# Performance work log

Hardware: AMD Instinct MI355X
Metric: run time of the kernel (lower is better)

The kernel has to match this reference:

```python
import jax, jax.numpy as jnp
import numpy as np

B, T, HW = 4, 27, 224
DIM, HEADS, LAYERS, MLP, NCLS, SEQ = 256, 4, 7, 512, 101, 56 * 56
HEAD_DIM = DIM // HEADS


def ste_sign(x):
    # binarize to {-1,0,+1} via sign() with straight-through gradient (matches torch .data mutation)
    return x + jax.lax.stop_gradient(jnp.sign(x) - x)


def layer_norm(x, s, b, eps=1e-5):
    m = x.mean(-1, keepdims=True)
    v = ((x - m) ** 2).mean(-1, keepdims=True)
    return (x - m) / jnp.sqrt(v + eps) * s + b


def conv3d(x, w, stride, pad):
    return jax.lax.conv_general_dilated(x, w, stride, [(p, p) for p in pad],
                                        dimension_numbers=('NCDHW', 'OIDHW', 'NCDHW'))


def encoder_layer(xx, p):
    l1s, l1b, qw, qb, pw, pb, l2s, l2b, f1w, f1b, f2w, f2b = p
    h = layer_norm(xx, l1s, l1b)
    qkv = jnp.einsum('bnd,ed->bne', h, qw) + qb  # (B, SEQ, 3*DIM)
    q, k, v = [t.reshape(B, SEQ, HEADS, HEAD_DIM).transpose(0, 2, 1, 3)
               for t in jnp.split(qkv, 3, axis=-1)]
    attn = jax.nn.softmax(jnp.einsum('bhnd,bhmd->bhnm', q, k) * HEAD_DIM ** -0.5, axis=-1)
    o = jnp.einsum('bhnm,bhmd->bhnd', attn, v).transpose(0, 2, 1, 3).reshape(B, SEQ, DIM)
    xx = xx + jnp.einsum('bnd,ed->bne', o, pw) + pb
    h = layer_norm(xx, l2s, l2b)
    h = jax.nn.gelu(jnp.einsum('bnd,ed->bne', h, f1w) + f1b, approximate=False)
    return xx + jnp.einsum('bne,de->bnd', h, f2w) + f2b, None


def forward(x, w1, w2, w3, tok_w, pos_emb, ln1_s, ln1_b, qkv_w, qkv_b, proj_w, proj_b,
            ln2_s, ln2_b, fc1_w, fc1_b, fc2_w, fc2_b, lnf_s, lnf_b, pool_w, pool_b,
            head_w, head_b, remat=False):
    st, pd = (3, 1, 1), (1, 3, 3)
    # BinarizeConv3d chain: first conv sees raw 3-channel input; later convs binarize their input
    h = jax.nn.relu(conv3d(x, ste_sign(w1), st, pd))            # (B,64,9,224,224)
    h = jax.nn.relu(conv3d(ste_sign(h), ste_sign(w2), st, pd))  # (B,32,3,224,224)
    h = jax.nn.relu(conv3d(ste_sign(h), ste_sign(w3), st, pd))  # (B,3,1,224,224)
    h = h.reshape(B, 3, HW, HW)
    # CCT tokenizer: Conv2d(3,256,k7,s2,p3,bias=False) + ReLU + MaxPool(3,2,1)
    t = jax.nn.relu(jax.lax.conv_general_dilated(h, tok_w, (2, 2), [(3, 3), (3, 3)],
                                                 dimension_numbers=('NCHW', 'OIHW', 'NCHW')))
    t = jax.lax.reduce_window(t, -jnp.inf, jax.lax.max, (1, 1, 3, 3), (1, 1, 2, 2),
                              ((0, 0), (0, 0), (1, 1), (1, 1)))  # (B,256,56,56)
    z = t.reshape(B, DIM, SEQ).transpose(0, 2, 1) + pos_emb      # (B,3136,256)
    body = jax.checkpoint(encoder_layer) if remat else encoder_layer
    z, _ = jax.lax.scan(body, z, (ln1_s, ln1_b, qkv_w, qkv_b, proj_w, proj_b,
                                  ln2_s, ln2_b, fc1_w, fc1_b, fc2_w, fc2_b))
    z = layer_norm(z, lnf_s, lnf_b)
    # sequence pooling: softmax(Linear(dim,1)) over tokens, weighted sum, then classifier
    a = jax.nn.softmax(z @ pool_w + pool_b, axis=1)  # (B, SEQ)
    pooled = jnp.einsum('bn,bnd->bd', a, z)
    return pooled @ head_w.T + head_b                # (B, 101)


def setup_inputs() -> dict:
    key = jax.random.key(0)
    ks = jax.random.split(key, 12)
    r = lambda k, s, sc=0.02: jax.random.normal(k, s, jnp.float32) * sc
    return {
        'x': jax.random.normal(ks[0], (B, 3, T, HW, HW), jnp.float32),
        'w1': r(ks[1], (64, 3, 3, 7, 7), 1.0),
        'w2': r(ks[2], (32, 64, 3, 7, 7), 1.0),
        'w3': r(ks[3], (3, 32, 3, 7, 7), 1.0),
        'tok_w': r(ks[4], (DIM, 3, 7, 7)),
        'pos_emb': r(ks[5], (1, SEQ, DIM), 0.2),
        'ln1_s': jnp.ones((LAYERS, DIM)), 'ln1_b': jnp.zeros((LAYERS, DIM)),
        'qkv_w': r(ks[6], (LAYERS, 3 * DIM, DIM)), 'qkv_b': jnp.zeros((LAYERS, 3 * DIM)),
        'proj_w': r(ks[7], (LAYERS, DIM, DIM)), 'proj_b': jnp.zeros((LAYERS, DIM)),
        'ln2_s': jnp.ones((LAYERS, DIM)), 'ln2_b': jnp.zeros((LAYERS, DIM)),
        'fc1_w': r(ks[8], (LAYERS, MLP, DIM)), 'fc1_b': jnp.zeros((LAYERS, MLP)),
        'fc2_w': r(ks[9], (LAYERS, DIM, MLP)), 'fc2_b': jnp.zeros((LAYERS, DIM)),
        'lnf_s': jnp.ones((DIM,)), 'lnf_b': jnp.zeros((DIM,)),
        'pool_w': r(ks[10], (DIM,)), 'pool_b': jnp.zeros((1,)),
        'head_w': r(ks[11], (NCLS, DIM)), 'head_b': jnp.zeros((NCLS,)),
    }


def reference(x, w1, w2, w3, tok_w, pos_emb, ln1_s, ln1_b, qkv_w, qkv_b, proj_w, proj_b,
              ln2_s, ln2_b, fc1_w, fc1_b, fc2_w, fc2_b, lnf_s, lnf_b, pool_w, pool_b,
              head_w, head_b):
    return forward(x, w1, w2, w3, tok_w, pos_emb, ln1_s, ln1_b, qkv_w, qkv_b, proj_w,
                   proj_b, ln2_s, ln2_b, fc1_w, fc1_b, fc2_w, fc2_b, lnf_s, lnf_b,
                   pool_w, pool_b, head_w, head_b)
```

## Files before the change

kernel.cpp:

```cpp
#include <hip/hip_runtime.h>
#include <hip/hip_bf16.h>
#include <cstdint>

#define SEQL 3136

typedef __attribute__((ext_vector_type(8))) short v8s;
typedef __attribute__((ext_vector_type(4))) float f32x4;
typedef __attribute__((ext_vector_type(4))) int v4i;

__device__ __forceinline__ uint16_t bf16u(float f) {
    uint32_t u = __float_as_uint(f);
    uint32_t r = u + 0x7fff + ((u >> 16) & 1);
    return (uint16_t)(r >> 16);
}
__device__ __forceinline__ float bf2f(uint16_t b) {
    uint32_t u = ((uint32_t)b) << 16;
    return __uint_as_float(u);
}

__global__ __launch_bounds__(256) void k_prep(const float* __restrict__ qw,
                                              const float* __restrict__ pw,
                                              const float* __restrict__ f1,
                                              const float* __restrict__ f2,
                                              const float* __restrict__ w1,
                                              const float* __restrict__ w2,
                                              const float* __restrict__ w3,
                                              uint16_t* __restrict__ dq,
                                              uint16_t* __restrict__ dp,
                                              uint16_t* __restrict__ d1,
                                              uint16_t* __restrict__ d2,
                                              uint16_t* __restrict__ w1b,
                                              uint64_t* __restrict__ wp2,
                                              uint64_t* __restrict__ wn2,
                                              uint32_t* __restrict__ wp3,
                                              uint32_t* __restrict__ wn3,
                                              uint32_t* __restrict__ w2i,
                                              uint16_t* __restrict__ w1f) {
    int gid = blockIdx.x * 256 + threadIdx.x;
    if (gid < 1376256) { dq[gid] = bf16u(qw[gid]); return; }
    if (gid < 1835008) { int i = gid - 1376256; dp[i] = bf16u(pw[i]); return; }
    if (gid < 2752512) { int i = gid - 1835008; d1[i] = bf16u(f1[i]); return; }
    if (gid < 3670016) { int i = gid - 2752512; d2[i] = bf16u(f2[i]); return; }
    if (gid < 3698688) {
        int i = gid - 3670016;
        int c = i & 63, oc = (i >> 6) & 63, kw = i >> 12;
        uint16_t v = 0;
        if (c < 63) {
            int ic = c / 21, rem = c % 21, kd = rem / 7, kh = rem % 7;
            float w = w1[((((oc * 3 + ic) * 3 + kd) * 7 + kh) * 7) + kw];
            v = (w > 0.f) ? 0x3F80 : ((w < 0.f) ? 0xBF80 : 0);
        }
        w1b[i] = v;
        return;
    }
    if (gid < 3703392) {
        int i = gid - 3698688;
        int oc = i / 147, r = i % 147;
        uint64_t p = 0, n = 0;
        for (int ic = 0; ic < 64; ic++) {
            float v = w2[(long)oc * 9408 + (long)ic * 147 + r];
            if (v > 0.f) p |= (1ull << ic);
            else if (v < 0.f) n |= (1ull << ic);
        }
        wp2[i] = p; wn2[i] = n;
        return;
    }
    if (gid < 3703833) {
        int i = gid - 3703392;
        int oc = i / 147, r = i % 147;
        uint32_t p = 0, n = 0;
        for (int ic = 0; ic < 32; ic++) {
            float v = w3[(long)oc * 4704 + (long)ic * 147 + r];
            if (v > 0.f) p |= (1u << ic);
            else if (v < 0.f) n |= (1u << ic);
        }
        wp3[i] = p; wn3[i] = n;
        return;
    }
    if (gid < 3779097) {
        int j = gid - 3703833;
        int s4 = (j & 3) * 4;
        int lane = (j >> 2) & 63;
        int nt = (j >> 8) & 1;
        int r = j >> 9;
        int g = lane >> 4, tl = lane & 15;
        int oc = nt * 16 + tl;
        uint32_t out = 0;
        for (int bb = 0; bb < 4; bb++) {
            int ic = g * 16 + s4 + bb;
            float w = w2[(long)oc * 9408 + (long)ic * 147 + r];
            uint32_t s8 = (w > 0.f) ? 0x01u : ((w < 0.f) ? 0xFFu : 0x00u);
            out |= s8 << (8 * bb);
        }
        w2i[j] = out;
        return;
    }
    if (gid < 3807769) {
        int i = gid - 3779097;
        int e = i & 7;
        int lane = (i >> 3) & 63;
        int f = (i >> 9) & 1;
        int wn = (i >> 10) & 1;
        int ks = (i >> 11) & 1;
        int kw = i >> 12;
        int tl = lane & 15, g = lane >> 4;
        int oc = wn * 32 + f * 16 + tl;
        int c = ks * 32 + g * 8 + e;
        uint16_t v = 0;
        if (c < 63) {
            int ic = c / 21, rem = c % 21, kd = rem / 7, kh = rem % 7;
            float w = w1[((((oc * 3 + ic) * 3 + kd) * 7 + kh) * 7) + kw];
            v = (w > 0.f) ? 0x3F80 : ((w < 0.f) ? 0xBF80 : 0);
        }
        w1f[i] = v;
    }
}

__global__ __launch_bounds__(256) void k_prepx(const float* __restrict__ x,
                                               uint32_t* __restrict__ X3) {
    int gid = blockIdx.x * 256 + threadIdx.x;
    if (gid >= 26158464) return;
    int iwp = gid % 116;
    int t = gid / 116;
    int ihp = t % 232; t /= 232;
    int dslot = t % 27; t /= 27;
    int ic = t % 3; t /= 3;
    int b = t & 3; int s = t >> 2;
    int d = dslot - 1;
    int ih = ihp - 3;
    uint32_t out = 0;
    if (d >= 0 && (unsigned)ih < 224u) {
        const float* xp = x + ((long)(b * 3 + ic) * 27 + d) * 50176 + ih * 224;
#pragma unroll
        for (int half = 0; half < 2; half++) {
            int iw = 2 * iwp + half - 3;
            float v = ((unsigned)iw < 224u) ? xp[iw] : 0.f;
            uint16_t hi = bf16u(v);
            uint16_t o = hi;
            if (s > 0) {
                float r1 = v - bf2f(hi);
                uint16_t lo = bf16u(r1);
                o = (s == 2) ? bf16u(r1 - bf2f(lo)) : lo;
            }
            out |= ((uint32_t)o) << (16 * half);
        }
    }
    X3[gid] = out;
}

__device__ __forceinline__ v8s ldA76(const uint16_t* Xt, int colb, int c0) {
    union { v8s v; uint2 u[2]; } t;
    const uint16_t* p = Xt + colb * 76 + c0;
    t.u[0] = *(const uint2*)p;
    t.u[1] = *(const uint2*)(p + 4);
    return t.v;
}

__global__ __launch_bounds__(256) void k_conv1m(const uint16_t* __restrict__ X3,
                                                const uint16_t* __restrict__ w1f,
                                                uint64_t* __restrict__ b1p) {
    __shared__ __align__(16) uint16_t Xt[232 * 76];
    __shared__ __align__(16) uint16_t Wb[2][4096];
    int tid = threadIdx.x;
    int bidx = blockIdx.x;
    int oh = (bidx & 7) * 28 + (bidx >> 3);
    int od = blockIdx.y, b = blockIdx.z;
    int lane = tid & 63, wv = tid >> 6;
    int wm = wv >> 1, wn = wv & 1;
    int tl = lane & 15, g = lane >> 4;

    f32x4 acc[7][2];
#pragma unroll
    for (int mt = 0; mt < 7; mt++) {
        acc[mt][0] = (f32x4){0.f, 0.f, 0.f, 0.f};
        acc[mt][1] = (f32x4){0.f, 0.f, 0.f, 0.f};
    }

    for (int s = 0; s < 3; s++) {
        if (tid < 232) {
            const uint16_t* Xb = X3 + ((long)(s * 4 + b) * 81 + (long)od * 3) * 53824
                               + oh * 232 + tid;
#pragma unroll
            for (int cp = 0; cp < 32; cp++) {
                const int c0 = 2 * cp, c1 = c0 + 1;
                uint32_t v0 = 0, v1 = 0;
                if (c0 < 63) {
                    const int ickd = c0 / 7, kh = c0 % 7;
                    const int ic = ickd / 3, kd = ickd % 3;
                    v0 = Xb[(long)(ic * 27 + kd) * 53824 + kh * 232];
                }
                if (c1 < 63) {
                    const int ickd = c1 / 7, kh = c1 % 7;
                    const int ic = ickd / 3, kd = ickd % 3;
                    v1 = Xb[(long)(ic * 27 + kd) * 53824 + kh * 232];
                }
                *(uint32_t*)&Xt[tid * 76 + c0] = v0 | (v1 << 16);
            }
        }
        {
            const uint4* src = (const uint4*)w1f;
            uint4* dst = (uint4*)Wb[0];
            dst[tid] = src[tid];
            dst[256 + tid] = src[256 + tid];
        }
        __syncthreads();
        for (int kw = 0; kw < 7; kw++) {
            int cur = kw & 1;
            if (kw < 6) {
                const uint4* src = (const uint4*)(w1f + (kw + 1) * 4096);
                uint4* dst = (uint4*)Wb[cur ^ 1];
                dst[tid] = src[tid];
                dst[256 + tid] = src[256 + tid];
            }
#pragma unroll
            for (int ks = 0; ks < 2; ks++) {
                const uint16_t* wfb = &Wb[cur][((ks * 2 + wn) * 2) * 512 + lane * 8];
                v8s b0 = *(const v8s*)wfb;
                v8s b1 = *(const v8s*)(wfb + 512);
#pragma unroll
                for (int mt = 0; mt < 7; mt++) {
                    int colb = (wm * 7 + mt) * 16 + tl + kw;
                    v8s a = ldA76(Xt, colb, ks * 32 + g * 8);
                    acc[mt][0] = __builtin_amdgcn_mfma_f32_16x16x32_bf16(a, b0, acc[mt][0], 0, 0, 0);
                    acc[mt][1] = __builtin_amdgcn_mfma_f32_16x16x32_bf16(a, b1, acc[mt][1], 0, 0, 0);
                }
            }
            __syncthreads();
        }
    }
    uint16_t* obits16 = (uint16_t*)Wb[1];
#pragma unroll
    for (int mt = 0; mt < 7; mt++)
#pragma unroll
        for (int nt = 0; nt < 2; nt++)
#pragma unroll
            for (int r = 0; r < 4; r++) {
                unsigned long long mask = __ballot(acc[mt][nt][r] > 0.f);
                if (tl == 0) {
                    int ow = (wm * 7 + mt) * 16 + g * 4 + r;
                    obits16[ow * 4 + wn * 2 + nt] = (uint16_t)(mask >> (g * 16));
                }
            }
    __syncthreads();
    if (tid < 224) {
        uint64_t w = (uint64_t)obits16[tid * 4]
                   | ((uint64_t)obits16[tid * 4 + 1] << 16)
                   | ((uint64_t)obits16[tid * 4 + 2] << 32)
                   | ((uint64_t)obits16[tid * 4 + 3] << 48);
        b1p[(((long)b * 9 + od) * 224 + oh) * 224 + tid] = w;
    }
}

__global__ __launch_bounds__(256) void k_conv2m(const uint64_t* __restrict__ bp1,
                                                const uint8_t* __restrict__ w2i,
                                                uint32_t* __restrict__ b2p) {
    __shared__ __align__(16) uint64_t xs[21 * 232];
    __shared__ uint16_t obits16[224 * 2];
    int tid = threadIdx.x;
    int bidx = blockIdx.x;
    int oh = (bidx & 7) * 28 + (bidx >> 3);
    int od = blockIdx.y, b = blockIdx.z;
    int lane = tid & 63, wv = tid >> 6;
    int tl = lane & 15, g = lane >> 4;
    int g2 = g >> 1, sh = (g & 1) * 16;

    for (int i = tid; i < 21 * 232; i += 256) {
        int row = i / 232, wp = i - row * 232;
        int kd = row / 7, kh = row - kd * 7;
        int d = od * 3 - 1 + kd;
        int h = oh - 3 + kh;
        int w = wp - 3;
        uint64_t v = 0;
        if ((unsigned)d < 9u && (unsigned)h < 224u && (unsigned)w < 224u)
            v = bp1[(((long)b * 9 + d) * 224 + h) * 224 + w];
        xs[i] = v;
    }

    int nmt = (wv < 2) ? 4 : 3;
    v4i acc[4][2];
#pragma unroll
    for (int mi = 0; mi < 4; mi++) {
        acc[mi][0] = (v4i){0, 0, 0, 0};
        acc[mi][1] = (v4i){0, 0, 0, 0};
    }
    __syncthreads();

    for (int row = 0; row < 21; row++) {
        const uint8_t* wr = w2i + (long)row * 14336;
        const uint32_t* x32 = (const uint32_t*)&xs[row * 232];
#pragma unroll
        for (int kw = 0; kw < 7; kw++) {
            v4i bf0 = *(const v4i*)&wr[(kw * 2 + 0) * 1024 + lane * 16];
            v4i bf1 = *(const v4i*)&wr[(kw * 2 + 1) * 1024 + lane * 16];
#pragma unroll
            for (int mi = 0; mi < 4; mi++) {
                if (mi < nmt) {
                    int mt = wv + mi * 4;
                    uint32_t c = x32[(mt * 16 + tl + kw) * 2 + g2] >> sh;
                    v4i a;
#pragma unroll
                    for (int j = 0; j < 4; j++) {
                        uint32_t d4 = (c >> (4 * j)) & 0xFu;
                        a[j] = (int)((d4 * 0x204081u) & 0x01010101u);
                    }
                    acc[mi][0] = __builtin_amdgcn_mfma_i32_16x16x64_i8(a, bf0, acc[mi][0], 0, 0, 0);
                    acc[mi][1] = __builtin_amdgcn_mfma_i32_16x16x64_i8(a, bf1, acc[mi][1], 0, 0, 0);
                }
            }
        }
    }
#pragma unroll
    for (int mi = 0; mi < 4; mi++) {
        if (mi < nmt) {
            int mt = wv + mi * 4;
#pragma unroll
            for (int nt = 0; nt < 2; nt++)
#pragma unroll
                for (int r = 0; r < 4; r++) {
                    unsigned long long mask = __ballot(acc[mi][nt][r] > 0);
                    if (tl == 0)
                        obits16[(mt * 16 + g * 4 + r) * 2 + nt] = (uint16_t)(mask >> (g * 16));
                }
        }
    }
    __syncthreads();
    if (tid < 224) {
        uint32_t wo = (uint32_t)obits16[tid * 2] | ((uint32_t)obits16[tid * 2 + 1] << 16);
        b2p[(((long)b * 3 + od) * 224 + oh) * 224 + tid] = wo;
    }
}

__global__ __launch_bounds__(256) void k_conv3(const uint32_t* __restrict__ bp2,
                                               const uint32_t* __restrict__ wp,
                                               const uint32_t* __restrict__ wn,
                                               float* __restrict__ h3) {
    int gid = blockIdx.x * 256 + threadIdx.x;
    int q = gid;
    int ow = q % 224; q /= 224;
    int oh = q % 224; q /= 224;
    int oc = q % 3;   int b = q / 3;
    int acc = 0;
    for (int kd = 0; kd < 3; kd++) {
        int d = kd - 1;
        if ((unsigned)d >= 3u) continue;
        for (int kh = 0; kh < 7; kh++) {
            int h = oh - 3 + kh;
            if ((unsigned)h >= 224u) continue;
            const uint32_t* bp = bp2 + ((long)(b * 3 + d) * 224 + h) * 224;
            const uint32_t* mp = wp + ((oc * 3 + kd) * 7 + kh) * 7;
            const uint32_t* mn = wn + ((oc * 3 + kd) * 7 + kh) * 7;
#pragma unroll
            for (int kw = 0; kw < 7; kw++) {
                int w = ow - 3 + kw;
                if ((unsigned)w < 224u) {
                    uint32_t bits = bp[w];
                    acc += __popc(bits & mp[kw]) - __popc(bits & mn[kw]);
                }
            }
        }
    }
    h3[gid] = fmaxf((float)acc, 0.f);
}

__global__ __launch_bounds__(256) void k_tok(const float* __restrict__ h3,
                                             const float* __restrict__ wt,
                                             float* __restrict__ tok) {
    __shared__ float xs[3 * 7 * 232];
    int tid = threadIdx.x;
    int oh = blockIdx.x, b = blockIdx.y;
    for (int i = tid; i < 3 * 7 * 232; i += 256) {
        int col = i % 232; int t = i / 232;
        int kh = t % 7; int ic = t / 7;
        int ih = oh * 2 - 3 + kh;
        int iw = col - 3;
        float v = 0.f;
        if ((unsigned)ih < 224u && (unsigned)iw < 224u)
            v = h3[((long)(b * 3 + ic) * 50176) + ih * 224 + iw];
        xs[i] = v;
    }
    __syncthreads();
    int oc = tid;
    float* obase = tok + ((long)(b * 112 + oh) * 112) * 256 + oc;
    for (int chunk = 0; chunk < 4; chunk++) {
        int ow0 = chunk * 28;
        float acc[28];
#pragma unroll
        for (int o2 = 0; o2 < 28; o2++) acc[o2] = 0.f;
        for (int ic = 0; ic < 3; ic++) {
#pragma unroll
            for (int kh = 0; kh < 7; kh++) {
                const float* row = &xs[(ic * 7 + kh) * 232 + ow0 * 2];
                float xv[61];
#pragma unroll
                for (int t = 0; t < 61; t++) xv[t] = row[t];
                const float* wr = wt + (oc * 3 + ic) * 49 + kh * 7;
                float w[7];
#pragma unroll
                for (int kw = 0; kw < 7; kw++) w[kw] = wr[kw];
#pragma unroll
                for (int kw = 0; kw < 7; kw++)
#pragma unroll
                    for (int o2 = 0; o2 < 28; o2++)
                        acc[o2] = fmaf(w[kw], xv[2 * o2 + kw], acc[o2]);
            }
        }
#pragma unroll
        for (int o2 = 0; o2 < 28; o2++)
            obase[(long)(ow0 + o2) * 256] = fmaxf(acc[o2], 0.f);
    }
}

__global__ __launch_bounds__(256) void k_pool_z(const float* __restrict__ tok,
                                                const float* __restrict__ pos,
                                                float* __restrict__ z) {
    int gid = blockIdx.x * 256 + threadIdx.x;
    int c = gid & 255;
    int n = (gid >> 8) % SEQL;
    int b = gid / (256 * SEQL);
    int oh = n / 56, ow = n % 56;
    const float* tp = tok + ((long)b * 112 * 112) * 256 + c;
    float m = -1e30f;
#pragma unroll
    for (int kh = 0; kh < 3; kh++) {
        int h = oh * 2 - 1 + kh;
        if ((unsigned)h >= 112u) continue;
#pragma unroll
        for (int kw = 0; kw < 3; kw++) {
            int w = ow * 2 - 1 + kw;
            if ((unsigned)w < 112u) m = fmaxf(m, tp[(long)(h * 112 + w) * 256]);
        }
    }
    z[gid] = m + pos[n * 256 + c];
}

__global__ __launch_bounds__(256) void k_gemm_ln(const float* __restrict__ Z,
                                                 const uint16_t* __restrict__ W,
                                                 const float* __restrict__ lns,
                                                 const float* __restrict__ lnb,
                                                 const float* __restrict__ bias,
                                                 uint16_t* __restrict__ C,
                                                 uint16_t* __restrict__ VT,
                                                 int N, int dogelu, int dovt) {
    __shared__ uint16_t As[128 * 40], Bs[128 * 40];
    __shared__ float mu[128], rsd[128];
    int tid = threadIdx.x;
    int lane = tid & 63, wave = tid >> 6;
    int wm = wave >> 1, wn = wave & 1;
    int m0 = blockIdx.y * 128, n0 = blockIdx.x * 128;
    {
        int row = tid >> 1, hf = tid & 1;
        const float* zr = Z + (long)(m0 + row) * 256 + hf * 128;
        float s = 0.f, sq = 0.f;
        for (int i = 0; i < 128; i++) { float v = zr[i]; s += v; sq += v * v; }
        s += __shfl_xor(s, 1); sq += __shfl_xor(sq, 1);
        if (hf == 0) {
            float m = s * (1.0f / 256.0f);
            mu[row] = m;
            rsd[row] = rsqrtf(sq * (1.0f / 256.0f) - m * m + 1e-5f);
        }
    }
    f32x4 acc[4][4];
#pragma unroll
    for (int i = 0; i < 4; i++)
#pragma unroll
        for (int j = 0; j < 4; j++) acc[i][j] = (f32x4){0.f, 0.f, 0.f, 0.f};
    int rl = lane & 15, kq = (lane >> 4) * 8;
    for (int k0 = 0; k0 < 256; k0 += 32) {
        __syncthreads();
#pragma unroll
        for (int c2 = 0; c2 < 16; c2++) {
            int idx = c2 * 256 + tid;
            int col = idx & 31, row = idx >> 5;
            float v = Z[(long)(m0 + row) * 256 + k0 + col];
            v = (v - mu[row]) * rsd[row] * lns[k0 + col] + lnb[k0 + col];
            As[row * 40 + col] = bf16u(v);
        }
#pragma unroll
        for (int c = 0; c < 2; c++) {
            int idx = c * 256 + tid;
            int row = idx >> 2, k8 = (idx & 3) * 8;
            *(uint4*)&Bs[row * 40 + k8] = *(const uint4*)&W[(long)(n0 + row) * 256 + k0 + k8];
        }
        __syncthreads();
        v8s a[4], bb[4];
#pragma unroll
        for (int i = 0; i < 4; i++) a[i] = *(const v8s*)&As[(wm * 64 + i * 16 + rl) * 40 + kq];
#pragma unroll
        for (int j = 0; j < 4; j++) bb[j] = *(const v8s*)&Bs[(wn * 64 + j * 16 + rl) * 40 + kq];
#pragma unroll
        for (int i = 0; i < 4; i++)
#pragma unroll
            for (int j = 0; j < 4; j++)
                acc[i][j] = __builtin_amdgcn_mfma_f32_16x16x32_bf16(a[i], bb[j], acc[i][j], 0, 0, 0);
    }
    int rq = (lane >> 4) * 4;
    bool vt = (dovt != 0) && (n0 >= 512);
#pragma unroll
    for (int i = 0; i < 4; i++) {
#pragma unroll
        for (int j = 0; j < 4; j++) {
            int col = n0 + wn * 64 + j * 16 + rl;
            float bval = bias[col];
#pragma unroll
            for (int r = 0; r < 4; r++) {
                int row = m0 + wm * 64 + i * 16 + rq + r;
                float v = acc[i][j][r] + bval;
                if (dogelu) v = 0.5f * v * (1.0f + erff(v * 0.70710678118654752f));
                if (vt) {
                    int hv = col - 512;
                    int h = hv >> 6, d = hv & 63;
                    int bb2 = row / SEQL, nn = row - bb2 * SEQL;
                    VT[((long)(bb2 * 4 + h) * 64 + d) * SEQL + nn] = bf16u(v);
                } else {
                    C[(long)row * N + col] = bf16u(v);
                }
            }
        }
    }
}

__global__ __launch_bounds__(256) void k_gemm(const uint16_t* __restrict__ A,
                                              const uint16_t* __restrict__ W,
                                              const float* __restrict__ bias,
                                              float* __restrict__ C,
                                              int M, int N, int K) {
    __shared__ uint16_t As[128 * 40], Bs[128 * 40];
    int tid = threadIdx.x;
    int lane = tid & 63, wave = tid >> 6;
    int wm = wave >> 1, wn = wave & 1;
    int m0 = blockIdx.y * 128, n0 = blockIdx.x * 128;
    f32x4 acc[4][4];
#pragma unroll
    for (int i = 0; i < 4; i++)
#pragma unroll
        for (int j = 0; j < 4; j++) acc[i][j] = (f32x4){0.f, 0.f, 0.f, 0.f};
    int rl = lane & 15, kq = (lane >> 4) * 8;
    for (int k0 = 0; k0 < K; k0 += 32) {
        __syncthreads();
#pragma unroll
        for (int c = 0; c < 2; c++) {
            int idx = c * 256 + tid;
            int row = idx >> 2, k8 = (idx & 3) * 8;
            *(uint4*)&As[row * 40 + k8] = *(const uint4*)&A[(long)(m0 + row) * K + k0 + k8];
            *(uint4*)&Bs[row * 40 + k8] = *(const uint4*)&W[(long)(n0 + row) * K + k0 + k8];
        }
        __syncthreads();
        v8s a[4], bb[4];
#pragma unroll
        for (int i = 0; i < 4; i++) a[i] = *(const v8s*)&As[(wm * 64 + i * 16 + rl) * 40 + kq];
#pragma unroll
        for (int j = 0; j < 4; j++) bb[j] = *(const v8s*)&Bs[(wn * 64 + j * 16 + rl) * 40 + kq];
#pragma unroll
        for (int i = 0; i < 4; i++)
#pragma unroll
            for (int j = 0; j < 4; j++)
                acc[i][j] = __builtin_amdgcn_mfma_f32_16x16x32_bf16(a[i], bb[j], acc[i][j], 0, 0, 0);
    }
    int rq = (lane >> 4) * 4;
#pragma unroll
    for (int i = 0; i < 4; i++) {
#pragma unroll
        for (int j = 0; j < 4; j++) {
            int col = n0 + wn * 64 + j * 16 + rl;
            float bval = bias[col];
#pragma unroll
            for (int r = 0; r < 4; r++) {
                int row = m0 + wm * 64 + i * 16 + rq + r;
                C[(long)row * N + col] += acc[i][j][r] + bval;
            }
        }
    }
}

__global__ __launch_bounds__(256) void k_flash(const uint16_t* __restrict__ G,
                                               const uint16_t* __restrict__ VT,
                                               uint16_t* __restrict__ o) {
    __shared__ __align__(16) uint32_t Qs[64 * 36], Ks[64 * 36], Vt[64 * 36];
    __shared__ __align__(16) uint16_t Ps[64 * 72];
    int tid = threadIdx.x;
    int lane = tid & 63, wv = tid >> 6;
    int qt = blockIdx.x, h = blockIdx.y, b = blockIdx.z;
    long base = (long)b * SEQL * 768 + h * 64;
    long vtbase = ((long)(b * 4 + h) * 64) * SEQL;
#pragma unroll
    for (int it = 0; it < 2; it++) {
        int idx = it * 256 + tid;
        int q8 = idx & 7, r = idx >> 3;
        *(uint4*)&Qs[r * 36 + q8 * 4] = *(const uint4*)&G[base + (long)(qt * 64 + r) * 768 + q8 * 8];
    }
    int g = lane >> 4, tl = lane & 15;
    int qr0 = wv * 16;
    __syncthreads();
    v8s aq[2];
#pragma unroll
    for (int ks = 0; ks < 2; ks++)
        aq[ks] = *(const v8s*)&Qs[(qr0 + tl) * 36 + ks * 16 + g * 4];

    float m_[4], l_[4];
    f32x4 ov[4];
#pragma unroll
    for (int r = 0; r < 4; r++) { m_[r] = -1e30f; l_[r] = 0.f; }
#pragma unroll
    for (int j = 0; j < 4; j++) ov[j] = (f32x4){0.f, 0.f, 0.f, 0.f};

    for (int kt = 0; kt < 49; kt++) {
        __syncthreads();
#pragma unroll
        for (int it = 0; it < 2; it++) {
            int idx = it * 256 + tid;
            int q8 = idx & 7, r = idx >> 3;
            *(uint4*)&Ks[r * 36 + q8 * 4] =
                *(const uint4*)&G[base + (long)(kt * 64 + r) * 768 + 256 + q8 * 8];
        }
#pragma unroll
        for (int it = 0; it < 2; it++) {
            int idx = it * 256 + tid;
            int r8 = idx & 7, d = idx >> 3;
            *(uint4*)&Vt[d * 36 + r8 * 4] =
                *(const uint4*)&VT[vtbase + (long)d * SEQL + kt * 64 + r8 * 8];
        }
        __syncthreads();
        f32x4 s[4];
#pragma unroll
        for (int j = 0; j < 4; j++) s[j] = (f32x4){0.f, 0.f, 0.f, 0.f};
#pragma unroll
        for (int ks = 0; ks < 2; ks++) {
#pragma unroll
            for (int j = 0; j < 4; j++) {
                v8s bk = *(const v8s*)&Ks[(j * 16 + tl) * 36 + ks * 16 + g * 4];
                s[j] = __builtin_amdgcn_mfma_f32_16x16x32_bf16(aq[ks], bk, s[j], 0, 0, 0);
            }
        }
        float alpha[4];
#pragma unroll
        for (int r = 0; r < 4; r++) {
            float s0 = s[0][r] * 0.125f, s1 = s[1][r] * 0.125f;
            float s2 = s[2][r] * 0.125f, s3 = s[3][r] * 0.125f;
            s[0][r] = s0; s[1][r] = s1; s[2][r] = s2; s[3][r] = s3;
            float mx = fmaxf(fmaxf(s0, s1), fmaxf(s2, s3));
#pragma unroll
            for (int off = 1; off < 16; off <<= 1) mx = fmaxf(mx, __shfl_xor(mx, off));
            float nm = fmaxf(m_[r], mx);
            alpha[r] = __expf(m_[r] - nm);
            float rs = 0.f;
#pragma unroll
            for (int j = 0; j < 4; j++) {
                float p = __expf(s[j][r] - nm);
                s[j][r] = p; rs += p;
            }
#pragma unroll
            for (int off = 1; off < 16; off <<= 1) rs += __shfl_xor(rs, off);
            l_[r] = l_[r] * alpha[r] + rs;
            m_[r] = nm;
        }
#pragma unroll
        for (int j = 0; j < 4; j++)
#pragma unroll
            for (int r = 0; r < 4; r++) ov[j][r] *= alpha[r];
#pragma unroll
        for (int j = 0; j < 4; j++)
#pragma unroll
            for (int r = 0; r < 4; r++)
                Ps[(qr0 + g * 4 + r) * 72 + j * 16 + tl] = bf16u(s[j][r]);
#pragma unroll
        for (int ks = 0; ks < 2; ks++) {
            v8s ap = *(const v8s*)&Ps[(qr0 + tl) * 72 + ks * 32 + g * 8];
#pragma unroll
            for (int jd = 0; jd < 4; jd++) {
                v8s bv = *(const v8s*)&Vt[(jd * 16 + tl) * 36 + ks * 16 + g * 4];
                ov[jd] = __builtin_amdgcn_mfma_f32_16x16x32_bf16(ap, bv, ov[jd], 0, 0, 0);
            }
        }
    }
    long ob = ((long)b * SEQL + qt * 64) * 256 + h * 64;
#pragma unroll
    for (int r = 0; r < 4; r++) {
        float inv = 1.0f / l_[r];
        int row = qr0 + g * 4 + r;
#pragma unroll
        for (int jd = 0; jd < 4; jd++)
            o[ob + (long)row * 256 + jd * 16 + tl] = bf16u(ov[jd][r] * inv);
    }
}

__global__ __launch_bounds__(256) void k_tail_rows(const float* __restrict__ Z,
                                                   const float* __restrict__ g,
                                                   const float* __restrict__ be,
                                                   const float* __restrict__ pw,
                                                   const float* __restrict__ pb,
                                                   float* __restrict__ LG,
                                                   float* __restrict__ MU,
                                                   float* __restrict__ RS) {
    int tid = threadIdx.x;
    int wv = tid >> 6, lane = tid & 63;
    int b = blockIdx.y;
    int r0 = blockIdx.x * 64;
    const float* Zb = Z + (long)b * SEQL * 256;
    for (int r = r0 + wv; r < r0 + 64; r += 4) {
        const float* xr = Zb + (long)r * 256;
        float v0 = xr[lane], v1 = xr[lane + 64], v2 = xr[lane + 128], v3 = xr[lane + 192];
        float s = v0 + v1 + v2 + v3;
#pragma unroll
        for (int off = 1; off < 64; off <<= 1) s += __shfl_xor(s, off);
        float mean = s * (1.0f / 256.0f);
        float d0 = v0 - mean, d1 = v1 - mean, d2 = v2 - mean, d3 = v3 - mean;
        float sq = d0 * d0 + d1 * d1 + d2 * d2 + d3 * d3;
#pragma unroll
        for (int off = 1; off < 64; off <<= 1) sq += __shfl_xor(sq, off);
        float rs_ = rsqrtf(sq * (1.0f / 256.0f) + 1e-5f);
        float a = (d0 * rs_ * g[lane] + be[lane]) * pw[lane]
                + (d1 * rs_ * g[lane + 64] + be[lane + 64]) * pw[lane + 64]
                + (d2 * rs_ * g[lane + 128] + be[lane + 128]) * pw[lane + 128]
                + (d3 * rs_ * g[lane + 192] + be[lane + 192]) * pw[lane + 192];
#pragma unroll
        for (int off = 1; off < 64; off <<= 1) a += __shfl_xor(a, off);
        if (lane == 0) {
            LG[b * SEQL + r] = a + pb[0];
            MU[b * SEQL + r] = mean;
            RS[b * SEQL + r] = rs_;
        }
    }
}

__global__ __launch_bounds__(256) void k_tail_sm(const float* __restrict__ LG,
                                                 const float* __restrict__ MU,
                                                 float* __restrict__ RSW,
                                                 float* __restrict__ SB) {
    __shared__ float red[256];
    int b = blockIdx.x, tid = threadIdx.x;
    const float* lg = LG + (long)b * SEQL;
    const float* mu = MU + (long)b * SEQL;
    float* rw = RSW + (long)b * SEQL;
    float m = -1e30f;
    for (int i = tid; i < SEQL; i += 256) m = fmaxf(m, lg[i]);
    red[tid] = m; __syncthreads();
    for (int s = 128; s > 0; s >>= 1) {
        if (tid < s) red[tid] = fmaxf(red[tid], red[tid + s]);
        __syncthreads();
    }
    float M = red[0]; __syncthreads();
    float sum = 0.f;
    for (int i = tid; i < SEQL; i += 256) sum += expf(lg[i] - M);
    red[tid] = sum; __syncthreads();
    for (int s = 128; s > 0; s >>= 1) {
        if (tid < s) red[tid] += red[tid + s];
        __syncthreads();
    }
    float inv = 1.0f / red[0];
    __syncthreads();
    float pB = 0.f;
    for (int i = tid; i < SEQL; i += 256) {
        float p = expf(lg[i] - M) * inv;
        float rs_ = rw[i];
        pB += p * mu[i] * rs_;
        rw[i] = p * rs_;
    }
    red[tid] = pB; __syncthreads();
    for (int s = 128; s > 0; s >>= 1) {
        if (tid < s) red[tid] += red[tid + s];
        __syncthreads();
    }
    if (tid == 0) SB[b] = red[0];
}

__global__ __launch_bounds__(256) void k_tail_gemv(const float* __restrict__ Z,
                                                   const float* __restrict__ RSW,
                                                   float* __restrict__ ACCP) {
    __shared__ float wsm[64];
    int b = blockIdx.y, tid = threadIdx.x;
    int n0 = blockIdx.x * 64;
    if (tid < 64) wsm[tid] = RSW[(long)b * SEQL + n0 + tid];
    __syncthreads();
    const float* Zb = Z + ((long)b * SEQL + n0) * 256;
    float acc = 0.f;
#pragma unroll 8
    for (int n = 0; n < 64; n++) acc = fmaf(wsm[n], Zb[(long)n * 256 + tid], acc);
    ACCP[((long)blockIdx.x * 4 + b) * 256 + tid] = acc;
}

__global__ __launch_bounds__(256) void k_tail_head(const float* __restrict__ ACCP,
                                                   const float* __restrict__ SB,
                                                   const float* __restrict__ g,
                                                   const float* __restrict__ be,
                                                   const float* __restrict__ hw,
                                                   const float* __restrict__ hb,
                                                   float* __restrict__ out) {
    __shared__ float pooled[256];
    int b = blockIdx.x, tid = threadIdx.x;
    float s = 0.f;
    for (int c = 0; c < 49; c++) s += ACCP[((long)c * 4 + b) * 256 + tid];
    pooled[tid] = g[tid] * (s - SB[b]) + be[tid];
    __syncthreads();
    if (tid < 101) {
        float a = hb[tid];
        for (int d = 0; d < 256; d++) a = fmaf(pooled[d], hw[tid * 256 + d], a);
        out[b * 101 + tid] = a;
    }
}

extern "C" void kernel_launch(void* const* d_in, const int* in_sizes, int n_in,
                              void* d_out, int out_size, void* d_ws, size_t ws_size,
                              hipStream_t stream) {
    (void)in_sizes; (void)n_in; (void)out_size; (void)ws_size;
    const float* x     = (const float*)d_in[0];
    const float* w1    = (const float*)d_in[1];
    const float* w2    = (const float*)d_in[2];
    const float* w3    = (const float*)d_in[3];
    const float* tokw  = (const float*)d_in[4];
    const float* pos   = (const float*)d_in[5];
    const float* ln1s  = (const float*)d_in[6];
    const float* ln1b  = (const float*)d_in[7];
    const float* qkvw  = (const float*)d_in[8];
    const float* qkvb  = (const float*)d_in[9];
    const float* projw = (const float*)d_in[10];
    const float* projb = (const float*)d_in[11];
    const float* ln2s  = (const float*)d_in[12];
    const float* ln2b  = (const float*)d_in[13];
    const float* fc1w  = (const float*)d_in[14];
    const float* fc1b  = (const float*)d_in[15];
    const float* fc2w  = (const float*)d_in[16];
    const float* fc2b  = (const float*)d_in[17];
    const float* lnfs  = (const float*)d_in[18];
    const float* lnfb  = (const float*)d_in[19];
    const float* poolw = (const float*)d_in[20];
    const float* poolb = (const float*)d_in[21];
    const float* headw = (const float*)d_in[22];
    const float* headb = (const float*)d_in[23];
    float* out = (float*)d_out;
    char* ws = (char*)d_ws;

    uint64_t* B1P = (uint64_t*)(ws + 0);
    uint32_t* B2P = (uint32_t*)(ws + 14450688);
    float*    H3  = (float*)(ws + 16859136);
    uint16_t* W1B = (uint16_t*)(ws + 19267584);
    uint64_t* WP2 = (uint64_t*)(ws + 19324928);
    uint64_t* WN2 = (uint64_t*)(ws + 19362560);
    uint32_t* WP3 = (uint32_t*)(ws + 19400192);
    uint32_t* WN3 = (uint32_t*)(ws + 19402240);
    uint16_t* WQb = (uint16_t*)(ws + 19404288);
    uint16_t* WPb = (uint16_t*)(ws + 22156800);
    uint16_t* W1b = (uint16_t*)(ws + 23074304);
    uint16_t* W2b = (uint16_t*)(ws + 24909312);
    uint16_t* X3  = (uint16_t*)(ws + 26744320);
    float*    TOK = (float*)(ws + 26744320);
    float*    Z   = (float*)(ws + 78124544);
    uint16_t* Gbf = (uint16_t*)(ws + 90969600);
    uint16_t* Obf = (uint16_t*)(ws + 110237184);
    uint16_t* MLPb= (uint16_t*)(ws + 116659712);
    uint16_t* VT  = (uint16_t*)(ws + 129504768);
    uint8_t*  W2I = (uint8_t*)(ws + 131378176);
    uint16_t* W1F = (uint16_t*)(ws + 131679232);
    float* LG   = (float*)(ws + 26744320);
    float* MU   = (float*)(ws + 26794496);
    float* RSW  = (float*)(ws + 26844672);
    float* SB   = (float*)(ws + 26894848);
    float* ACCP = (float*)(ws + 26894912);

    k_prep<<<14875, 256, 0, stream>>>(qkvw, projw, fc1w, fc2w, w1, w2, w3,
                                      WQb, WPb, W1b, W2b, W1B, WP2, WN2, WP3, WN3,
                                      (uint32_t*)W2I, W1F);
    k_prepx<<<102182, 256, 0, stream>>>(x, (uint32_t*)X3);

    k_conv1m<<<dim3(224, 9, 4), 256, 0, stream>>>(X3, W1F, B1P);
    k_conv2m<<<dim3(224, 3, 4), 256, 0, stream>>>(B1P, W2I, B2P);
    k_conv3<<<2352, 256, 0, stream>>>(B2P, WP3, WN3, H3);
    k_tok<<<dim3(112, 4), 256, 0, stream>>>(H3, tokw, TOK);
    k_pool_z<<<12544, 256, 0, stream>>>(TOK, pos, Z);

    for (int l = 0; l < 7; l++) {
        k_gemm_ln<<<dim3(6, 98), 256, 0, stream>>>(Z, WQb + (long)l * 196608,
                                                   ln1s + l * 256, ln1b + l * 256,
                                                   qkvb + l * 768, Gbf, VT,
                                                   768, 0, 1);
        k_flash<<<dim3(49, 4, 4), 256, 0, stream>>>(Gbf, VT, Obf);
        k_gemm<<<dim3(2, 98), 256, 0, stream>>>(Obf, WPb + (long)l * 65536,
                                                projb + l * 256, Z,
                                                12544, 256, 256);
        k_gemm_ln<<<dim3(4, 98), 256, 0, stream>>>(Z, W1b + (long)l * 131072,
                                                   ln2s + l * 256, ln2b + l * 256,
                                                   fc1b + l * 512, MLPb, nullptr,
                                                   512, 1, 0);
        k_gemm<<<dim3(2, 98), 256, 0, stream>>>(MLPb, W2b + (long)l * 131072,
                                                fc2b + l * 256, Z,
                                                12544, 256, 512);
    }

    k_tail_rows<<<dim3(49, 4), 256, 0, stream>>>(Z, lnfs, lnfb, poolw, poolb,
                                                 LG, MU, RSW);
    k_tail_sm<<<4, 256, 0, stream>>>(LG, MU, RSW, SB);
    k_tail_gemv<<<dim3(49, 4), 256, 0, stream>>>(Z, RSW, ACCP);
    k_tail_head<<<4, 256, 0, stream>>>(ACCP, SB, lnfs, lnfb, headw, headb, out);
}
```

Baseline: 3.106 ms.

## Double-buffer K/V tiles in flash attention and fold softmax scale into Q

The flash attention kernel now double-buffers the K and V shared-memory tiles, prefetching the next tile while computing the current one. This cuts the two barriers per iteration down to one. The P staging buffer now reuses the Q shared-memory region, so LDS use stays about the same. The 1/8 attention scale is applied to Q in the QKV GEMM epilogue rather than to every score, which changes bf16 rounding slightly. The prefetch is a plain synchronous global-to-LDS copy, so overlap depends on the compiler and scheduler hiding the latency.

After: 3.277 ms. 1.06x slower.

```diff
diff --git a/kernel.cpp b/kernel.cpp
--- a/kernel.cpp
+++ b/kernel.cpp
@@ -506,6 +506,7 @@
                 int row = m0 + wm * 64 + i * 16 + rq + r;
                 float v = acc[i][j][r] + bval;
                 if (dogelu) v = 0.5f * v * (1.0f + erff(v * 0.70710678118654752f));
+                if (dovt != 0 && col < 256) v *= 0.125f;
                 if (vt) {
                     int hv = col - 512;
                     int h = hv >> 6, d = hv & 63;
@@ -575,8 +576,8 @@
 __global__ __launch_bounds__(256) void k_flash(const uint16_t* __restrict__ G,
                                                const uint16_t* __restrict__ VT,
                                                uint16_t* __restrict__ o) {
-    __shared__ __align__(16) uint32_t Qs[64 * 36], Ks[64 * 36], Vt[64 * 36];
-    __shared__ __align__(16) uint16_t Ps[64 * 72];
+    __shared__ __align__(16) uint32_t QP[64 * 36];
+    __shared__ __align__(16) uint32_t Ks[2][64 * 36], Vt[2][64 * 36];
     int tid = threadIdx.x;
     int lane = tid & 63, wv = tid >> 6;
     int qt = blockIdx.x, h = blockIdx.y, b = blockIdx.z;
@@ -586,7 +587,21 @@
     for (int it = 0; it < 2; it++) {
         int idx = it * 256 + tid;
         int q8 = idx & 7, r = idx >> 3;
-        *(uint4*)&Qs[r * 36 + q8 * 4] = *(const uint4*)&G[base + (long)(qt * 64 + r) * 768 + q8 * 8];
+        *(uint4*)&QP[r * 36 + q8 * 4] = *(const uint4*)&G[base + (long)(qt * 64 + r) * 768 + q8 * 8];
+    }
+#pragma unroll
+    for (int it = 0; it < 2; it++) {
+        int idx = it * 256 + tid;
+        int q8 = idx & 7, r = idx >> 3;
+        *(uint4*)&Ks[0][r * 36 + q8 * 4] =
+            *(const uint4*)&G[base + (long)r * 768 + 256 + q8 * 8];
+    }
+#pragma unroll
+    for (int it = 0; it < 2; it++) {
+        int idx = it * 256 + tid;
+        int r8 = idx & 7, d = idx >> 3;
+        *(uint4*)&Vt[0][d * 36 + r8 * 4] =
+            *(const uint4*)&VT[vtbase + (long)d * SEQL + r8 * 8];
     }
     int g = lane >> 4, tl = lane & 15;
     int qr0 = wv * 16;
@@ -594,7 +609,9 @@
     v8s aq[2];
 #pragma unroll
     for (int ks = 0; ks < 2; ks++)
-        aq[ks] = *(const v8s*)&Qs[(qr0 + tl) * 36 + ks * 16 + g * 4];
+        aq[ks] = *(const v8s*)&QP[(qr0 + tl) * 36 + ks * 16 + g * 4];
+    __syncthreads();
+    uint16_t* Ps = (uint16_t*)QP;
 
     float m_[4], l_[4];
     f32x4 ov[4];
@@ -604,22 +621,24 @@
     for (int j = 0; j < 4; j++) ov[j] = (f32x4){0.f, 0.f, 0.f, 0.f};
 
     for (int kt = 0; kt < 49; kt++) {
-        __syncthreads();
-#pragma unroll
-        for (int it = 0; it < 2; it++) {
-            int idx = it * 256 + tid;
-            int q8 = idx & 7, r = idx >> 3;
-            *(uint4*)&Ks[r * 36 + q8 * 4] =
-                *(const uint4*)&G[base + (long)(kt * 64 + r) * 768 + 256 + q8 * 8];
-        }
-#pragma unroll
-        for (int it = 0; it < 2; it++) {
-            int idx = it * 256 + tid;
-            int r8 = idx & 7, d = idx >> 3;
-            *(uint4*)&Vt[d * 36 + r8 * 4] =
-                *(const uint4*)&VT[vtbase + (long)d * SEQL + kt * 64 + r8 * 8];
-        }
-        __syncthreads();
+        int cur = kt & 1;
+        if (kt < 48) {
+            int nk = kt + 1;
+#pragma unroll
+            for (int it = 0; it < 2; it++) {
+                int idx = it * 256 + tid;
+                int q8 = idx & 7, r = idx >> 3;
+                *(uint4*)&Ks[cur ^ 1][r * 36 + q8 * 4] =
+                    *(const uint4*)&G[base + (long)(nk * 64 + r) * 768 + 256 + q8 * 8];
+            }
+#pragma unroll
+            for (int it = 0; it < 2; it++) {
+                int idx = it * 256 + tid;
+                int r8 = idx & 7, d = idx >> 3;
+                *(uint4*)&Vt[cur ^ 1][d * 36 + r8 * 4] =
+                    *(const uint4*)&VT[vtbase + (long)d * SEQL + nk * 64 + r8 * 8];
+            }
+        }
         f32x4 s[4];
 #pragma unroll
         for (int j = 0; j < 4; j++) s[j] = (f32x4){0.f, 0.f, 0.f, 0.f};
@@ -627,16 +646,15 @@
         for (int ks = 0; ks < 2; ks++) {
 #pragma unroll
             for (int j = 0; j < 4; j++) {
-                v8s bk = *(const v8s*)&Ks[(j * 16 + tl) * 36 + ks * 16 + g * 4];
+                v8s bk = *(const v8s*)&Ks[cur][(j * 16 + tl) * 36 + ks * 16 + g * 4];
                 s[j] = __builtin_amdgcn_mfma_f32_16x16x32_bf16(aq[ks], bk, s[j], 0, 0, 0);
             }
         }
         float alpha[4];
 #pragma unroll
         for (int r = 0; r < 4; r++) {
-            float s0 = s[0][r] * 0.125f, s1 = s[1][r] * 0.125f;
-            float s2 = s[2][r] * 0.125f, s3 = s[3][r] * 0.125f;
-            s[0][r] = s0; s[1][r] = s1; s[2][r] = s2; s[3][r] = s3;
+            float s0 = s[0][r], s1 = s[1][r];
+            float s2 = s[2][r], s3 = s[3][r];
             float mx = fmaxf(fmaxf(s0, s1), fmaxf(s2, s3));
 #pragma unroll
             for (int off = 1; off < 16; off <<= 1) mx = fmaxf(mx, __shfl_xor(mx, off));
@@ -667,10 +685,11 @@
             v8s ap = *(const v8s*)&Ps[(qr0 + tl) * 72 + ks * 32 + g * 8];
 #pragma unroll
             for (int jd = 0; jd < 4; jd++) {
-                v8s bv = *(const v8s*)&Vt[(jd * 16 + tl) * 36 + ks * 16 + g * 4];
+                v8s bv = *(const v8s*)&Vt[cur][(jd * 16 + tl) * 36 + ks * 16 + g * 4];
                 ov[jd] = __builtin_amdgcn_mfma_f32_16x16x32_bf16(ap, bv, ov[jd], 0, 0, 0);
             }
         }
+        __syncthreads();
     }
     long ob = ((long)b * SEQL + qt * 64) * 256 + h * 64;
 #pragma unroll
```
